# Kernel optimization log

Measured on AMD Instinct MI355X. Metric: run time of the kernel, lower is better.

The kernel has to match this reference:

```python
import jax, jax.numpy as jnp
import numpy as np

B, T, IN, H, OUT, L = 64, 4096, 32, 128, 32, 2


def setup_inputs() -> dict:
    key = jax.random.key(0)
    ks = jax.random.split(key, 12)
    s = 1.0 / np.sqrt(H)
    inp = {"x": jax.random.normal(ks[0], (B, T, IN), dtype=jnp.float32)}
    # layer 0 (input_dim -> H), layer 1 (H -> H); PyTorch GRU layout: [3H, in] with gates (r, z, n)
    inp["W_ih0"] = jax.random.uniform(ks[1], (3 * H, IN), jnp.float32, -s, s)
    inp["W_hh0"] = jax.random.uniform(ks[2], (3 * H, H), jnp.float32, -s, s)
    inp["b_ih0"] = jax.random.uniform(ks[3], (3 * H,), jnp.float32, -s, s)
    inp["b_hh0"] = jax.random.uniform(ks[4], (3 * H,), jnp.float32, -s, s)
    inp["W_ih1"] = jax.random.uniform(ks[5], (3 * H, H), jnp.float32, -s, s)
    inp["W_hh1"] = jax.random.uniform(ks[6], (3 * H, H), jnp.float32, -s, s)
    inp["b_ih1"] = jax.random.uniform(ks[7], (3 * H,), jnp.float32, -s, s)
    inp["b_hh1"] = jax.random.uniform(ks[8], (3 * H,), jnp.float32, -s, s)
    inp["fc_w"] = jax.random.uniform(ks[9], (OUT, H), jnp.float32, -s, s)
    inp["fc_b"] = jax.random.uniform(ks[10], (OUT,), jnp.float32, -s, s)
    return inp


def _gru_layer(x_seq, W_ih, W_hh, b_ih, b_hh):
    # x_seq: [B, T, in]; precompute the input projection as one big GEMM
    gi = jnp.einsum("bti,gi->btg", x_seq, W_ih) + b_ih  # [B, T, 3H]
    h0 = jnp.zeros((x_seq.shape[0], W_hh.shape[1]), x_seq.dtype)

    def step(h, gi_t):
        gh = h @ W_hh.T + b_hh  # [B, 3H]
        i_r, i_z, i_n = jnp.split(gi_t, 3, axis=-1)
        h_r, h_z, h_n = jnp.split(gh, 3, axis=-1)
        r = jax.nn.sigmoid(i_r + h_r)
        z = jax.nn.sigmoid(i_z + h_z)
        n = jnp.tanh(i_n + r * h_n)
        h_new = (1.0 - z) * n + z * h
        return h_new, h_new

    hT, outs = jax.lax.scan(step, h0, jnp.swapaxes(gi, 0, 1))  # outs: [T, B, H]
    return jnp.swapaxes(outs, 0, 1), hT


def reference(x, W_ih0, W_hh0, b_ih0, b_hh0, W_ih1, W_hh1, b_ih1, b_hh1, fc_w, fc_b):
    y0, h0 = _gru_layer(x, W_ih0, W_hh0, b_ih0, b_hh0)
    y1, h1 = _gru_layer(y0, W_ih1, W_hh1, b_ih1, b_hh1)
    out = jnp.einsum("bth,oh->bto", y1, fc_w) + fc_b  # [B, T, OUT]
    h = jnp.stack([h0, h1], axis=0)  # [n_layers, B, H]
    return out, h
```

## Files before the change

### kernel.cpp

```cpp
#include <hip/hip_runtime.h>

#define BB 64
#define TT 4096
#define IN0 32
#define HH 128
#define G3 384
#define NOUT 32
#define RING 64
#define CH 8

typedef _Float16 h2 __attribute__((ext_vector_type(2)));
typedef _Float16 h8 __attribute__((ext_vector_type(8)));
union H8 { h8 v; h2 p[4]; };

struct SM {
    float pg[G3 * 5];
    float pgi[G3 * 5];
    float hs[2][HH];
    _Float16 hf[2][HH];
    _Float16 xh[2][IN0];
    _Float16 ys[CH][HH];
    float bias1[G3];
    float bias2[G3];
    float fcw[NOUT * 129];
    float fcb[NOUT];
    float pfc[NOUT * 9];
};

__device__ __forceinline__ float fast_sigmoid(float x) {
    x = fminf(fmaxf(x, -30.f), 30.f);
    float e = __expf(-x);
    return __builtin_amdgcn_rcpf(1.f + e);
}
__device__ __forceinline__ float fast_tanh(float x) {
    x = fminf(fmaxf(x, -15.f), 15.f);
    float e = __expf(-2.f * x);
    return (1.f - e) * __builtin_amdgcn_rcpf(1.f + e);
}
__device__ __forceinline__ float fdot2(h2 a, h2 b, float c) {
#if __has_builtin(__builtin_amdgcn_fdot2)
    return __builtin_amdgcn_fdot2(a, b, c, false);
#else
    return fmaf((float)a.x, (float)b.x, fmaf((float)a.y, (float)b.y, c));
#endif
}
__device__ __forceinline__ int aload(const int* p) {
    return __hip_atomic_load(p, __ATOMIC_RELAXED, __HIP_MEMORY_SCOPE_AGENT);
}
__device__ __forceinline__ void astore(int* p, int v) {
    __hip_atomic_store(p, v, __ATOMIC_RELAXED, __HIP_MEMORY_SCOPE_AGENT);
}
__device__ __forceinline__ h2 cvt2(float a, float b) {
    h2 r; r.x = (_Float16)a; r.y = (_Float16)b; return r;
}

__device__ void role_A(SM& sm, const float* __restrict__ xb,
                       const float* __restrict__ W_ih, const float* __restrict__ W_hh,
                       const float* __restrict__ b_ih, const float* __restrict__ b_hh,
                       _Float16* __restrict__ y0b, float* __restrict__ hout, int* flagA)
{
    const int tid = threadIdx.x;
    const int rp = tid % 192, kq = tid / 192;
    const int r0 = 2 * rp, r1 = r0 + 1;
    const int pA0 = r0 * 5 + kq, pA1 = r1 * 5 + kq;

    h2 wh0[16], wh1[16], wi0[4], wi1[4];
    #pragma unroll
    for (int i = 0; i < 16; ++i) {
        float2 f0 = *(const float2*)&W_hh[r0 * HH + kq * 32 + 2 * i];
        float2 f1 = *(const float2*)&W_hh[r1 * HH + kq * 32 + 2 * i];
        wh0[i] = cvt2(f0.x, f0.y); wh1[i] = cvt2(f1.x, f1.y);
    }
    #pragma unroll
    for (int i = 0; i < 4; ++i) {
        float2 f0 = *(const float2*)&W_ih[r0 * IN0 + kq * 8 + 2 * i];
        float2 f1 = *(const float2*)&W_ih[r1 * IN0 + kq * 8 + 2 * i];
        wi0[i] = cvt2(f0.x, f0.y); wi1[i] = cvt2(f1.x, f1.y);
    }
    for (int i = tid; i < G3; i += 768) { sm.bias1[i] = b_ih[i]; sm.bias2[i] = b_hh[i]; }
    if (tid < HH) { sm.hs[0][tid] = 0.f; sm.hf[0][tid] = (_Float16)0.f; }
    if (tid < 8) {
        float4 f = ((const float4*)xb)[tid];
        ((h2*)&sm.xh[0][0])[2 * tid]     = cvt2(f.x, f.y);
        ((h2*)&sm.xh[0][0])[2 * tid + 1] = cvt2(f.z, f.w);
    }
    __syncthreads();

    int cur = 0;
    for (int t = 0; t < TT; ++t) {
        float4 pf;
        if (tid >= 128 && tid < 136) {
            int tn = (t + 1 < TT) ? t + 1 : t;
            pf = ((const float4*)(xb + (size_t)tn * IN0))[tid - 128];
        }
        const h8* hv = (const h8*)&sm.hf[cur][kq * 32];
        float a0 = 0.f, a1 = 0.f;
        #pragma unroll
        for (int i = 0; i < 4; ++i) {
            H8 hh; hh.v = hv[i];
            #pragma unroll
            for (int j = 0; j < 4; ++j) {
                a0 = fdot2(wh0[4 * i + j], hh.p[j], a0);
                a1 = fdot2(wh1[4 * i + j], hh.p[j], a1);
            }
        }
        sm.pg[pA0] = a0; sm.pg[pA1] = a1;
        H8 xx; xx.v = ((const h8*)&sm.xh[cur][0])[kq];
        float c0 = 0.f, c1 = 0.f;
        #pragma unroll
        for (int j = 0; j < 4; ++j) {
            c0 = fdot2(wi0[j], xx.p[j], c0);
            c1 = fdot2(wi1[j], xx.p[j], c1);
        }
        sm.pgi[pA0] = c0; sm.pgi[pA1] = c1;
        __syncthreads();

        const int nxt = cur ^ 1;
        if (tid < HH) {
            const int j = tid;
            float gir = sm.pgi[j*5+0]+sm.pgi[j*5+1]+sm.pgi[j*5+2]+sm.pgi[j*5+3] + sm.bias1[j];
            float giz = sm.pgi[(j+HH)*5+0]+sm.pgi[(j+HH)*5+1]+sm.pgi[(j+HH)*5+2]+sm.pgi[(j+HH)*5+3] + sm.bias1[j+HH];
            float gin = sm.pgi[(j+2*HH)*5+0]+sm.pgi[(j+2*HH)*5+1]+sm.pgi[(j+2*HH)*5+2]+sm.pgi[(j+2*HH)*5+3] + sm.bias1[j+2*HH];
            float ghr = sm.pg[j*5+0]+sm.pg[j*5+1]+sm.pg[j*5+2]+sm.pg[j*5+3] + sm.bias2[j];
            float ghz = sm.pg[(j+HH)*5+0]+sm.pg[(j+HH)*5+1]+sm.pg[(j+HH)*5+2]+sm.pg[(j+HH)*5+3] + sm.bias2[j+HH];
            float ghn = sm.pg[(j+2*HH)*5+0]+sm.pg[(j+2*HH)*5+1]+sm.pg[(j+2*HH)*5+2]+sm.pg[(j+2*HH)*5+3] + sm.bias2[j+2*HH];
            float rg = fast_sigmoid(gir + ghr);
            float zg = fast_sigmoid(giz + ghz);
            float ng = fast_tanh(gin + rg * ghn);
            float hn = (1.f - zg) * ng + zg * sm.hs[cur][j];
            sm.hs[nxt][j] = hn;
            sm.hf[nxt][j] = (_Float16)hn;
            y0b[(size_t)t * HH + j] = (_Float16)hn;
            if (t == TT - 1) hout[j] = hn;
        } else if (tid < 136) {
            int i = tid - 128;
            ((h2*)&sm.xh[nxt][0])[2 * i]     = cvt2(pf.x, pf.y);
            ((h2*)&sm.xh[nxt][0])[2 * i + 1] = cvt2(pf.z, pf.w);
        }
        __syncthreads();
        if ((t & 7) == 7 && tid == 0) { __threadfence(); astore(flagA, t + 1); }
        cur = nxt;
    }
}

__device__ void role_B(SM& sm, const _Float16* __restrict__ y0b,
                       const float* __restrict__ W_ih, const float* __restrict__ b_ih,
                       float* __restrict__ ring, int* flagA, int* flagB, int* flagC)
{
    const int tid = threadIdx.x;
    const int rp = tid % 192, kq = tid / 192;
    const int r0 = 2 * rp, r1 = r0 + 1;
    const int pA0 = r0 * 5 + kq, pA1 = r1 * 5 + kq;

    h2 wi0[16], wi1[16];
    #pragma unroll
    for (int i = 0; i < 16; ++i) {
        float2 f0 = *(const float2*)&W_ih[r0 * HH + kq * 32 + 2 * i];
        float2 f1 = *(const float2*)&W_ih[r1 * HH + kq * 32 + 2 * i];
        wi0[i] = cvt2(f0.x, f0.y); wi1[i] = cvt2(f1.x, f1.y);
    }
    for (int i = tid; i < G3; i += 768) sm.bias1[i] = b_ih[i];

    for (int T0 = 0; T0 < TT; T0 += CH) {
        if (tid == 0) {
            while (aload(flagA) < T0 + CH) __builtin_amdgcn_s_sleep(2);
            int need = T0 + CH - RING;
            while (aload(flagC) < need) __builtin_amdgcn_s_sleep(2);
            __threadfence();
        }
        __syncthreads();
        for (int i = tid; i < CH * HH / 2; i += 768)
            ((unsigned*)sm.ys)[i] = ((const unsigned*)(y0b + (size_t)T0 * HH))[i];
        __syncthreads();
        for (int s = 0; s < CH; ++s) {
            const h8* yv = (const h8*)&sm.ys[s][kq * 32];
            float a0 = 0.f, a1 = 0.f;
            #pragma unroll
            for (int i = 0; i < 4; ++i) {
                H8 yy; yy.v = yv[i];
                #pragma unroll
                for (int j = 0; j < 4; ++j) {
                    a0 = fdot2(wi0[4 * i + j], yy.p[j], a0);
                    a1 = fdot2(wi1[4 * i + j], yy.p[j], a1);
                }
            }
            sm.pg[pA0] = a0; sm.pg[pA1] = a1;
            __syncthreads();
            if (tid < G3) {
                float sum = sm.pg[tid*5+0]+sm.pg[tid*5+1]+sm.pg[tid*5+2]+sm.pg[tid*5+3] + sm.bias1[tid];
                ring[(size_t)((T0 + s) & (RING - 1)) * G3 + tid] = sum;
            }
            __syncthreads();
        }
        if (tid == 0) { __threadfence(); astore(flagB, T0 + CH); }
    }
}

__device__ void role_C(SM& sm, const float* __restrict__ ring,
                       const float* __restrict__ W_hh, const float* __restrict__ b_hh,
                       const float* __restrict__ fc_w, const float* __restrict__ fc_b,
                       float* __restrict__ outb, float* __restrict__ hout,
                       int* flagB, int* flagC)
{
    const int tid = threadIdx.x;
    const int rp = tid % 192, kq = tid / 192;
    const int r0 = 2 * rp, r1 = r0 + 1;
    const int pA0 = r0 * 5 + kq, pA1 = r1 * 5 + kq;

    h2 wh0[16], wh1[16];
    #pragma unroll
    for (int i = 0; i < 16; ++i) {
        float2 f0 = *(const float2*)&W_hh[r0 * HH + kq * 32 + 2 * i];
        float2 f1 = *(const float2*)&W_hh[r1 * HH + kq * 32 + 2 * i];
        wh0[i] = cvt2(f0.x, f0.y); wh1[i] = cvt2(f1.x, f1.y);
    }
    if (tid == 0) astore(flagC, 0);
    for (int i = tid; i < G3; i += 768) sm.bias2[i] = b_hh[i];
    for (int i = tid; i < NOUT * HH; i += 768)
        sm.fcw[(i >> 7) * 129 + (i & 127)] = fc_w[i];
    if (tid < NOUT) sm.fcb[tid] = fc_b[tid];
    if (tid < HH) { sm.hs[0][tid] = 0.f; sm.hf[0][tid] = (_Float16)0.f; }
    __syncthreads();

    int cur = 0;
    for (int t = 0; t < TT; ++t) {
        if ((t & 7) == 0) {
            if (tid == 0) {
                while (aload(flagB) < t + CH) __builtin_amdgcn_s_sleep(2);
                __threadfence();
            }
            __syncthreads();
        }
        if (t >= 2 && tid >= 704 && tid < 736) {
            int o = tid - 704;
            float s = sm.fcb[o];
            #pragma unroll
            for (int j = 0; j < 8; ++j) s += sm.pfc[o * 9 + j];
            outb[(size_t)(t - 2) * NOUT + o] = s;
        }
        float gir = 0.f, giz = 0.f, gin = 0.f;
        if (tid < HH) {
            const float* rr = ring + (size_t)(t & (RING - 1)) * G3;
            gir = rr[tid]; giz = rr[tid + HH]; gin = rr[tid + 2 * HH];
        }
        const h8* hv = (const h8*)&sm.hf[cur][kq * 32];
        float a0 = 0.f, a1 = 0.f;
        #pragma unroll
        for (int i = 0; i < 4; ++i) {
            H8 hh; hh.v = hv[i];
            #pragma unroll
            for (int j = 0; j < 4; ++j) {
                a0 = fdot2(wh0[4 * i + j], hh.p[j], a0);
                a1 = fdot2(wh1[4 * i + j], hh.p[j], a1);
            }
        }
        sm.pg[pA0] = a0; sm.pg[pA1] = a1;
        __syncthreads();

        const int nxt = cur ^ 1;
        if (tid < HH) {
            const int j = tid;
            float ghr = sm.pg[j*5+0]+sm.pg[j*5+1]+sm.pg[j*5+2]+sm.pg[j*5+3] + sm.bias2[j];
            float ghz = sm.pg[(j+HH)*5+0]+sm.pg[(j+HH)*5+1]+sm.pg[(j+HH)*5+2]+sm.pg[(j+HH)*5+3] + sm.bias2[j+HH];
            float ghn = sm.pg[(j+2*HH)*5+0]+sm.pg[(j+2*HH)*5+1]+sm.pg[(j+2*HH)*5+2]+sm.pg[(j+2*HH)*5+3] + sm.bias2[j+2*HH];
            float rg = fast_sigmoid(gir + ghr);
            float zg = fast_sigmoid(giz + ghz);
            float ng = fast_tanh(gin + rg * ghn);
            float hn = (1.f - zg) * ng + zg * sm.hs[cur][j];
            sm.hs[nxt][j] = hn;
            sm.hf[nxt][j] = (_Float16)hn;
            if (t == TT - 1) hout[j] = hn;
        }
        if (tid >= 384 && tid < 640) {
            int idx = tid - 384, o = idx & 31, ks = idx >> 5;
            const float* hv2 = &sm.hs[cur][ks * 16];
            const float* wv = &sm.fcw[o * 129 + ks * 16];
            float s = 0.f;
            #pragma unroll
            for (int i = 0; i < 16; ++i) s = fmaf(hv2[i], wv[i], s);
            sm.pfc[o * 9 + ks] = s;
        }
        __syncthreads();
        if ((t & 7) == 7 && tid == 0) { __threadfence(); astore(flagC, t + 1); }
        cur = nxt;
    }
    if (tid >= 704 && tid < 736) {
        int o = tid - 704;
        float s = sm.fcb[o];
        #pragma unroll
        for (int j = 0; j < 8; ++j) s += sm.pfc[o * 9 + j];
        outb[(size_t)(TT - 2) * NOUT + o] = s;
    }
    __syncthreads();
    if (tid >= 384 && tid < 640) {
        int idx = tid - 384, o = idx & 31, ks = idx >> 5;
        const float* hv2 = &sm.hs[cur][ks * 16];
        const float* wv = &sm.fcw[o * 129 + ks * 16];
        float s = 0.f;
        #pragma unroll
        for (int i = 0; i < 16; ++i) s = fmaf(hv2[i], wv[i], s);
        sm.pfc[o * 9 + ks] = s;
    }
    __syncthreads();
    if (tid >= 704 && tid < 736) {
        int o = tid - 704;
        float s = sm.fcb[o];
        #pragma unroll
        for (int j = 0; j < 8; ++j) s += sm.pfc[o * 9 + j];
        outb[(size_t)(TT - 1) * NOUT + o] = s;
    }
}

extern "C" __global__ void __launch_bounds__(768, 3)
gru_pipe_kernel(
    const float* x,
    const float* W_ih0, const float* W_hh0, const float* b_ih0, const float* b_hh0,
    const float* W_ih1, const float* W_hh1, const float* b_ih1, const float* b_hh1,
    const float* fc_w, const float* fc_b,
    float* out, float* hstack, _Float16* y0, float* ring, int* flags)
{
    __shared__ SM sm;
    const int wg = blockIdx.x;
    if (wg < BB) {
        const int b = wg;
        role_A(sm, x + (size_t)b * TT * IN0, W_ih0, W_hh0, b_ih0, b_hh0,
               y0 + (size_t)b * TT * HH, hstack + b * HH,
               &flags[(0 * 64 + b) * 16]);
    } else if (wg < 2 * BB) {
        const int b = wg - BB;
        role_B(sm, y0 + (size_t)b * TT * HH, W_ih1, b_ih1,
               ring + (size_t)b * RING * G3,
               &flags[(0 * 64 + b) * 16], &flags[(1 * 64 + b) * 16], &flags[(2 * 64 + b) * 16]);
    } else {
        const int b = wg - 2 * BB;
        role_C(sm, ring + (size_t)b * RING * G3, W_hh1, b_hh1, fc_w, fc_b,
               out + (size_t)b * TT * NOUT, hstack + BB * HH + b * HH,
               &flags[(1 * 64 + b) * 16], &flags[(2 * 64 + b) * 16]);
    }
}

extern "C" void kernel_launch(void* const* d_in, const int* in_sizes, int n_in,
                              void* d_out, int out_size, void* d_ws, size_t ws_size,
                              hipStream_t stream) {
    const float* x     = (const float*)d_in[0];
    const float* W_ih0 = (const float*)d_in[1];
    const float* W_hh0 = (const float*)d_in[2];
    const float* b_ih0 = (const float*)d_in[3];
    const float* b_hh0 = (const float*)d_in[4];
    const float* W_ih1 = (const float*)d_in[5];
    const float* W_hh1 = (const float*)d_in[6];
    const float* b_ih1 = (const float*)d_in[7];
    const float* b_hh1 = (const float*)d_in[8];
    const float* fc_w  = (const float*)d_in[9];
    const float* fc_b  = (const float*)d_in[10];

    float* out    = (float*)d_out;
    float* hstack = out + (size_t)BB * TT * NOUT;
    _Float16* y0  = (_Float16*)d_ws;
    float* ring   = (float*)((char*)d_ws + (68ull << 20));
    int* flags    = (int*)((char*)d_ws + (80ull << 20));

    gru_pipe_kernel<<<3 * BB, 768, 0, stream>>>(
        x, W_ih0, W_hh0, b_ih0, b_hh0,
        W_ih1, W_hh1, b_ih1, b_hh1,
        fc_w, fc_b, out, hstack, y0, ring, flags);
}
```

Measured before the change: 4.840 ms.

## Merge layer-1 input projection into recurrence block, one full gate row per thread

Removes the separate layer-1 input-projection role and its global ring buffer. Layer 1's recurrent blocks now compute both the W_ih and W_hh dot products themselves, reading y0 directly and waiting only on layer 0's progress flag. Each of 384 threads owns a full gate row, with 64 h2 weights held in registers per matrix, so the per-step K-split reduction through shared memory disappears. Block size drops from 768 to 384 threads and the grid from 192 to 128 blocks. The cost is much higher register pressure per thread and more serial dot-product work per thread on each step.

```diff
diff --git a/kernel.cpp b/kernel.cpp
--- a/kernel.cpp
+++ b/kernel.cpp
@@ -6,25 +6,18 @@
 #define HH 128
 #define G3 384
 #define NOUT 32
-#define RING 64
-#define CH 8
 
 typedef _Float16 h2 __attribute__((ext_vector_type(2)));
 typedef _Float16 h8 __attribute__((ext_vector_type(8)));
 union H8 { h8 v; h2 p[4]; };
 
 struct SM {
-    float pg[G3 * 5];
-    float pgi[G3 * 5];
+    float g[2 * HH];
+    float gin[HH];
+    float ghn[HH];
     float hs[2][HH];
     _Float16 hf[2][HH];
-    _Float16 xh[2][IN0];
-    _Float16 ys[CH][HH];
-    float bias1[G3];
-    float bias2[G3];
-    float fcw[NOUT * 129];
-    float fcb[NOUT];
-    float pfc[NOUT * 9];
+    float pfc[2][NOUT * 9];
 };
 
 __device__ __forceinline__ float fast_sigmoid(float x) {
@@ -60,282 +53,225 @@
                        _Float16* __restrict__ y0b, float* __restrict__ hout, int* flagA)
 {
     const int tid = threadIdx.x;
-    const int rp = tid % 192, kq = tid / 192;
-    const int r0 = 2 * rp, r1 = r0 + 1;
-    const int pA0 = r0 * 5 + kq, pA1 = r1 * 5 + kq;
-
-    h2 wh0[16], wh1[16], wi0[4], wi1[4];
-    #pragma unroll
-    for (int i = 0; i < 16; ++i) {
-        float2 f0 = *(const float2*)&W_hh[r0 * HH + kq * 32 + 2 * i];
-        float2 f1 = *(const float2*)&W_hh[r1 * HH + kq * 32 + 2 * i];
-        wh0[i] = cvt2(f0.x, f0.y); wh1[i] = cvt2(f1.x, f1.y);
-    }
-    #pragma unroll
-    for (int i = 0; i < 4; ++i) {
-        float2 f0 = *(const float2*)&W_ih[r0 * IN0 + kq * 8 + 2 * i];
-        float2 f1 = *(const float2*)&W_ih[r1 * IN0 + kq * 8 + 2 * i];
-        wi0[i] = cvt2(f0.x, f0.y); wi1[i] = cvt2(f1.x, f1.y);
-    }
-    for (int i = tid; i < G3; i += 768) { sm.bias1[i] = b_ih[i]; sm.bias2[i] = b_hh[i]; }
-    if (tid < HH) { sm.hs[0][tid] = 0.f; sm.hf[0][tid] = (_Float16)0.f; }
-    if (tid < 8) {
-        float4 f = ((const float4*)xb)[tid];
-        ((h2*)&sm.xh[0][0])[2 * tid]     = cvt2(f.x, f.y);
-        ((h2*)&sm.xh[0][0])[2 * tid + 1] = cvt2(f.z, f.w);
+    h2 wh[64], wi[16];
+    #pragma unroll
+    for (int k = 0; k < 64; ++k) {
+        float2 f = *(const float2*)&W_hh[tid * HH + 2 * k];
+        wh[k] = cvt2(f.x, f.y);
+    }
+    #pragma unroll
+    for (int k = 0; k < 16; ++k) {
+        float2 f = *(const float2*)&W_ih[tid * IN0 + 2 * k];
+        wi[k] = cvt2(f.x, f.y);
+    }
+    const bool is_n = tid >= 2 * HH;
+    const float bi = b_ih[tid], bh = b_hh[tid];
+    float hreg = 0.f;
+    if (tid < HH) sm.hf[0][tid] = (_Float16)0.f;
+
+    float4 pf[8];
+    #pragma unroll
+    for (int i = 0; i < 8; ++i) pf[i] = ((const float4*)xb)[i];
+    h2 xc[16];
+    #pragma unroll
+    for (int i = 0; i < 8; ++i) {
+        xc[2 * i]     = cvt2(pf[i].x, pf[i].y);
+        xc[2 * i + 1] = cvt2(pf[i].z, pf[i].w);
     }
     __syncthreads();
 
     int cur = 0;
     for (int t = 0; t < TT; ++t) {
-        float4 pf;
-        if (tid >= 128 && tid < 136) {
-            int tn = (t + 1 < TT) ? t + 1 : t;
-            pf = ((const float4*)(xb + (size_t)tn * IN0))[tid - 128];
-        }
-        const h8* hv = (const h8*)&sm.hf[cur][kq * 32];
-        float a0 = 0.f, a1 = 0.f;
-        #pragma unroll
-        for (int i = 0; i < 4; ++i) {
+        const int tn = (t + 1 < TT) ? t + 1 : t;
+        #pragma unroll
+        for (int i = 0; i < 8; ++i) pf[i] = ((const float4*)(xb + (size_t)tn * IN0))[i];
+
+        float ah0 = bh, ah1 = 0.f;
+        const h8* hv = (const h8*)&sm.hf[cur][0];
+        #pragma unroll
+        for (int i = 0; i < 16; ++i) {
             H8 hh; hh.v = hv[i];
             #pragma unroll
             for (int j = 0; j < 4; ++j) {
-                a0 = fdot2(wh0[4 * i + j], hh.p[j], a0);
-                a1 = fdot2(wh1[4 * i + j], hh.p[j], a1);
+                if (((4 * i + j) & 1) == 0) ah0 = fdot2(wh[4 * i + j], hh.p[j], ah0);
+                else                        ah1 = fdot2(wh[4 * i + j], hh.p[j], ah1);
             }
         }
-        sm.pg[pA0] = a0; sm.pg[pA1] = a1;
-        H8 xx; xx.v = ((const h8*)&sm.xh[cur][0])[kq];
-        float c0 = 0.f, c1 = 0.f;
-        #pragma unroll
-        for (int j = 0; j < 4; ++j) {
-            c0 = fdot2(wi0[j], xx.p[j], c0);
-            c1 = fdot2(wi1[j], xx.p[j], c1);
-        }
-        sm.pgi[pA0] = c0; sm.pgi[pA1] = c1;
+        float ai0 = bi, ai1 = 0.f;
+        #pragma unroll
+        for (int j = 0; j < 16; ++j) {
+            if (j & 1) ai1 = fdot2(wi[j], xc[j], ai1);
+            else       ai0 = fdot2(wi[j], xc[j], ai0);
+        }
+        const float sgh = ah0 + ah1, sgi = ai0 + ai1;
+        if (!is_n) sm.g[tid] = sgh + sgi;
+        else { sm.gin[tid - 2 * HH] = sgi; sm.ghn[tid - 2 * HH] = sgh; }
         __syncthreads();
 
-        const int nxt = cur ^ 1;
         if (tid < HH) {
-            const int j = tid;
-            float gir = sm.pgi[j*5+0]+sm.pgi[j*5+1]+sm.pgi[j*5+2]+sm.pgi[j*5+3] + sm.bias1[j];
-            float giz = sm.pgi[(j+HH)*5+0]+sm.pgi[(j+HH)*5+1]+sm.pgi[(j+HH)*5+2]+sm.pgi[(j+HH)*5+3] + sm.bias1[j+HH];
-            float gin = sm.pgi[(j+2*HH)*5+0]+sm.pgi[(j+2*HH)*5+1]+sm.pgi[(j+2*HH)*5+2]+sm.pgi[(j+2*HH)*5+3] + sm.bias1[j+2*HH];
-            float ghr = sm.pg[j*5+0]+sm.pg[j*5+1]+sm.pg[j*5+2]+sm.pg[j*5+3] + sm.bias2[j];
-            float ghz = sm.pg[(j+HH)*5+0]+sm.pg[(j+HH)*5+1]+sm.pg[(j+HH)*5+2]+sm.pg[(j+HH)*5+3] + sm.bias2[j+HH];
-            float ghn = sm.pg[(j+2*HH)*5+0]+sm.pg[(j+2*HH)*5+1]+sm.pg[(j+2*HH)*5+2]+sm.pg[(j+2*HH)*5+3] + sm.bias2[j+2*HH];
-            float rg = fast_sigmoid(gir + ghr);
-            float zg = fast_sigmoid(giz + ghz);
-            float ng = fast_tanh(gin + rg * ghn);
-            float hn = (1.f - zg) * ng + zg * sm.hs[cur][j];
-            sm.hs[nxt][j] = hn;
-            sm.hf[nxt][j] = (_Float16)hn;
-            y0b[(size_t)t * HH + j] = (_Float16)hn;
-            if (t == TT - 1) hout[j] = hn;
-        } else if (tid < 136) {
-            int i = tid - 128;
-            ((h2*)&sm.xh[nxt][0])[2 * i]     = cvt2(pf.x, pf.y);
-            ((h2*)&sm.xh[nxt][0])[2 * i + 1] = cvt2(pf.z, pf.w);
+            float rg = fast_sigmoid(sm.g[tid]);
+            float zg = fast_sigmoid(sm.g[tid + HH]);
+            float ng = fast_tanh(sm.gin[tid] + rg * sm.ghn[tid]);
+            hreg = (1.f - zg) * ng + zg * hreg;
+            sm.hf[cur ^ 1][tid] = (_Float16)hreg;
+            y0b[(size_t)t * HH + tid] = (_Float16)hreg;
+            if (t == TT - 1) hout[tid] = hreg;
+        }
+        #pragma unroll
+        for (int i = 0; i < 8; ++i) {
+            xc[2 * i]     = cvt2(pf[i].x, pf[i].y);
+            xc[2 * i + 1] = cvt2(pf[i].z, pf[i].w);
         }
         __syncthreads();
         if ((t & 7) == 7 && tid == 0) { __threadfence(); astore(flagA, t + 1); }
-        cur = nxt;
-    }
-}
-
-__device__ void role_B(SM& sm, const _Float16* __restrict__ y0b,
-                       const float* __restrict__ W_ih, const float* __restrict__ b_ih,
-                       float* __restrict__ ring, int* flagA, int* flagB, int* flagC)
+        cur ^= 1;
+    }
+}
+
+__device__ void role_C(SM& sm, const _Float16* __restrict__ yb,
+                       const float* __restrict__ W_ih, const float* __restrict__ W_hh,
+                       const float* __restrict__ b_ih, const float* __restrict__ b_hh,
+                       const float* __restrict__ fc_w, const float* __restrict__ fc_b,
+                       float* __restrict__ outb, float* __restrict__ hout, int* flagA)
 {
     const int tid = threadIdx.x;
-    const int rp = tid % 192, kq = tid / 192;
-    const int r0 = 2 * rp, r1 = r0 + 1;
-    const int pA0 = r0 * 5 + kq, pA1 = r1 * 5 + kq;
-
-    h2 wi0[16], wi1[16];
-    #pragma unroll
-    for (int i = 0; i < 16; ++i) {
-        float2 f0 = *(const float2*)&W_ih[r0 * HH + kq * 32 + 2 * i];
-        float2 f1 = *(const float2*)&W_ih[r1 * HH + kq * 32 + 2 * i];
-        wi0[i] = cvt2(f0.x, f0.y); wi1[i] = cvt2(f1.x, f1.y);
-    }
-    for (int i = tid; i < G3; i += 768) sm.bias1[i] = b_ih[i];
-
-    for (int T0 = 0; T0 < TT; T0 += CH) {
-        if (tid == 0) {
-            while (aload(flagA) < T0 + CH) __builtin_amdgcn_s_sleep(2);
-            int need = T0 + CH - RING;
-            while (aload(flagC) < need) __builtin_amdgcn_s_sleep(2);
-            __threadfence();
-        }
-        __syncthreads();
-        for (int i = tid; i < CH * HH / 2; i += 768)
-            ((unsigned*)sm.ys)[i] = ((const unsigned*)(y0b + (size_t)T0 * HH))[i];
-        __syncthreads();
-        for (int s = 0; s < CH; ++s) {
-            const h8* yv = (const h8*)&sm.ys[s][kq * 32];
-            float a0 = 0.f, a1 = 0.f;
-            #pragma unroll
-            for (int i = 0; i < 4; ++i) {
-                H8 yy; yy.v = yv[i];
-                #pragma unroll
-                for (int j = 0; j < 4; ++j) {
-                    a0 = fdot2(wi0[4 * i + j], yy.p[j], a0);
-                    a1 = fdot2(wi1[4 * i + j], yy.p[j], a1);
-                }
-            }
-            sm.pg[pA0] = a0; sm.pg[pA1] = a1;
-            __syncthreads();
-            if (tid < G3) {
-                float sum = sm.pg[tid*5+0]+sm.pg[tid*5+1]+sm.pg[tid*5+2]+sm.pg[tid*5+3] + sm.bias1[tid];
-                ring[(size_t)((T0 + s) & (RING - 1)) * G3 + tid] = sum;
-            }
-            __syncthreads();
-        }
-        if (tid == 0) { __threadfence(); astore(flagB, T0 + CH); }
-    }
-}
-
-__device__ void role_C(SM& sm, const float* __restrict__ ring,
-                       const float* __restrict__ W_hh, const float* __restrict__ b_hh,
-                       const float* __restrict__ fc_w, const float* __restrict__ fc_b,
-                       float* __restrict__ outb, float* __restrict__ hout,
-                       int* flagB, int* flagC)
-{
-    const int tid = threadIdx.x;
-    const int rp = tid % 192, kq = tid / 192;
-    const int r0 = 2 * rp, r1 = r0 + 1;
-    const int pA0 = r0 * 5 + kq, pA1 = r1 * 5 + kq;
-
-    h2 wh0[16], wh1[16];
-    #pragma unroll
-    for (int i = 0; i < 16; ++i) {
-        float2 f0 = *(const float2*)&W_hh[r0 * HH + kq * 32 + 2 * i];
-        float2 f1 = *(const float2*)&W_hh[r1 * HH + kq * 32 + 2 * i];
-        wh0[i] = cvt2(f0.x, f0.y); wh1[i] = cvt2(f1.x, f1.y);
-    }
-    if (tid == 0) astore(flagC, 0);
-    for (int i = tid; i < G3; i += 768) sm.bias2[i] = b_hh[i];
-    for (int i = tid; i < NOUT * HH; i += 768)
-        sm.fcw[(i >> 7) * 129 + (i & 127)] = fc_w[i];
-    if (tid < NOUT) sm.fcb[tid] = fc_b[tid];
-    if (tid < HH) { sm.hs[0][tid] = 0.f; sm.hf[0][tid] = (_Float16)0.f; }
+    h2 wh[64], wi[64];
+    #pragma unroll
+    for (int k = 0; k < 64; ++k) {
+        float2 f = *(const float2*)&W_hh[tid * HH + 2 * k]; wh[k] = cvt2(f.x, f.y);
+        float2 g = *(const float2*)&W_ih[tid * HH + 2 * k]; wi[k] = cvt2(g.x, g.y);
+    }
+    const bool is_n = tid >= 2 * HH;
+    const float bi = b_ih[tid], bh = b_hh[tid];
+    float hreg = 0.f;
+    const int fidx = tid - HH, fo = fidx & 31, fks = fidx >> 5;
+    float fw[16]; float fb = 0.f;
+    if (tid >= HH) {
+        #pragma unroll
+        for (int i = 0; i < 16; ++i) fw[i] = fc_w[fo * HH + fks * 16 + i];
+        if (tid < HH + NOUT) fb = fc_b[fo];
+    }
+    if (tid < HH) { sm.hf[0][tid] = (_Float16)0.f; sm.hs[0][tid] = 0.f; sm.hs[1][tid] = 0.f; }
+
+    if (tid == 0) {
+        while (aload(flagA) < 16) __builtin_amdgcn_s_sleep(8);
+        __threadfence();
+    }
     __syncthreads();
+    H8 yv[16];
+    #pragma unroll
+    for (int i = 0; i < 16; ++i) yv[i].v = ((const h8*)yb)[i];
 
     int cur = 0;
     for (int t = 0; t < TT; ++t) {
-        if ((t & 7) == 0) {
+        if (t && (t & 7) == 0) {
             if (tid == 0) {
-                while (aload(flagB) < t + CH) __builtin_amdgcn_s_sleep(2);
+                int tgt = t + 16; if (tgt > TT) tgt = TT;
+                while (aload(flagA) < tgt) __builtin_amdgcn_s_sleep(2);
                 __threadfence();
             }
             __syncthreads();
         }
-        if (t >= 2 && tid >= 704 && tid < 736) {
-            int o = tid - 704;
-            float s = sm.fcb[o];
-            #pragma unroll
-            for (int j = 0; j < 8; ++j) s += sm.pfc[o * 9 + j];
-            outb[(size_t)(t - 2) * NOUT + o] = s;
-        }
-        float gir = 0.f, giz = 0.f, gin = 0.f;
+
+        float ah0 = bh, ah1 = 0.f;
+        const h8* hv = (const h8*)&sm.hf[cur][0];
+        #pragma unroll
+        for (int i = 0; i < 16; ++i) {
+            H8 hh; hh.v = hv[i];
+            #pragma unroll
+            for (int j = 0; j < 4; ++j) {
+                if (((4 * i + j) & 1) == 0) ah0 = fdot2(wh[4 * i + j], hh.p[j], ah0);
+                else                        ah1 = fdot2(wh[4 * i + j], hh.p[j], ah1);
+            }
+        }
+        float ai0 = bi, ai1 = 0.f;
+        #pragma unroll
+        for (int i = 0; i < 16; ++i) {
+            #pragma unroll
+            for (int j = 0; j < 4; ++j) {
+                if (((4 * i + j) & 1) == 0) ai0 = fdot2(wi[4 * i + j], yv[i].p[j], ai0);
+                else                        ai1 = fdot2(wi[4 * i + j], yv[i].p[j], ai1);
+            }
+        }
+        const int tn = (t + 1 < TT) ? t + 1 : t;
+        const h8* ysrc = (const h8*)(yb + (size_t)tn * HH);
+        #pragma unroll
+        for (int i = 0; i < 16; ++i) yv[i].v = ysrc[i];
+
+        const float sgh = ah0 + ah1, sgi = ai0 + ai1;
+        if (!is_n) sm.g[tid] = sgh + sgi;
+        else { sm.gin[tid - 2 * HH] = sgi; sm.ghn[tid - 2 * HH] = sgh; }
+
+        if (tid >= HH) {
+            const float* hvv = &sm.hs[cur][fks * 16];
+            float s = 0.f;
+            #pragma unroll
+            for (int i = 0; i < 16; ++i) s = fmaf(fw[i], hvv[i], s);
+            sm.pfc[t & 1][fo * 9 + fks] = s;
+        }
+        if (t >= 2 && tid >= HH && tid < HH + NOUT) {
+            float s = fb;
+            #pragma unroll
+            for (int j = 0; j < 8; ++j) s += sm.pfc[(t - 1) & 1][fo * 9 + j];
+            outb[(size_t)(t - 2) * NOUT + fo] = s;
+        }
+        __syncthreads();
+
         if (tid < HH) {
-            const float* rr = ring + (size_t)(t & (RING - 1)) * G3;
-            gir = rr[tid]; giz = rr[tid + HH]; gin = rr[tid + 2 * HH];
-        }
-        const h8* hv = (const h8*)&sm.hf[cur][kq * 32];
-        float a0 = 0.f, a1 = 0.f;
-        #pragma unroll
-        for (int i = 0; i < 4; ++i) {
-            H8 hh; hh.v = hv[i];
-            #pragma unroll
-            for (int j = 0; j < 4; ++j) {
-                a0 = fdot2(wh0[4 * i + j], hh.p[j], a0);
-                a1 = fdot2(wh1[4 * i + j], hh.p[j], a1);
-            }
-        }
-        sm.pg[pA0] = a0; sm.pg[pA1] = a1;
+            float rg = fast_sigmoid(sm.g[tid]);
+            float zg = fast_sigmoid(sm.g[tid + HH]);
+            float ng = fast_tanh(sm.gin[tid] + rg * sm.ghn[tid]);
+            hreg = (1.f - zg) * ng + zg * hreg;
+            sm.hf[cur ^ 1][tid] = (_Float16)hreg;
+            sm.hs[cur ^ 1][tid] = hreg;
+            if (t == TT - 1) hout[tid] = hreg;
+        }
         __syncthreads();
-
-        const int nxt = cur ^ 1;
-        if (tid < HH) {
-            const int j = tid;
-            float ghr = sm.pg[j*5+0]+sm.pg[j*5+1]+sm.pg[j*5+2]+sm.pg[j*5+3] + sm.bias2[j];
-            float ghz = sm.pg[(j+HH)*5+0]+sm.pg[(j+HH)*5+1]+sm.pg[(j+HH)*5+2]+sm.pg[(j+HH)*5+3] + sm.bias2[j+HH];
-            float ghn = sm.pg[(j+2*HH)*5+0]+sm.pg[(j+2*HH)*5+1]+sm.pg[(j+2*HH)*5+2]+sm.pg[(j+2*HH)*5+3] + sm.bias2[j+2*HH];
-            float rg = fast_sigmoid(gir + ghr);
-            float zg = fast_sigmoid(giz + ghz);
-            float ng = fast_tanh(gin + rg * ghn);
-            float hn = (1.f - zg) * ng + zg * sm.hs[cur][j];
-            sm.hs[nxt][j] = hn;
-            sm.hf[nxt][j] = (_Float16)hn;
-            if (t == TT - 1) hout[j] = hn;
-        }
-        if (tid >= 384 && tid < 640) {
-            int idx = tid - 384, o = idx & 31, ks = idx >> 5;
-            const float* hv2 = &sm.hs[cur][ks * 16];
-            const float* wv = &sm.fcw[o * 129 + ks * 16];
-            float s = 0.f;
-            #pragma unroll
-            for (int i = 0; i < 16; ++i) s = fmaf(hv2[i], wv[i], s);
-            sm.pfc[o * 9 + ks] = s;
-        }
-        __syncthreads();
-        if ((t & 7) == 7 && tid == 0) { __threadfence(); astore(flagC, t + 1); }
-        cur = nxt;
-    }
-    if (tid >= 704 && tid < 736) {
-        int o = tid - 704;
-        float s = sm.fcb[o];
-        #pragma unroll
-        for (int j = 0; j < 8; ++j) s += sm.pfc[o * 9 + j];
-        outb[(size_t)(TT - 2) * NOUT + o] = s;
+        cur ^= 1;
+    }
+
+    if (tid >= HH && tid < HH + NOUT) {
+        float s = fb;
+        #pragma unroll
+        for (int j = 0; j < 8; ++j) s += sm.pfc[(TT - 1) & 1][fo * 9 + j];
+        outb[(size_t)(TT - 2) * NOUT + fo] = s;
+    }
+    if (tid >= HH) {
+        const float* hvv = &sm.hs[cur][fks * 16];
+        float s = 0.f;
+        #pragma unroll
+        for (int i = 0; i < 16; ++i) s = fmaf(fw[i], hvv[i], s);
+        sm.pfc[TT & 1][fo * 9 + fks] = s;
     }
     __syncthreads();
-    if (tid >= 384 && tid < 640) {
-        int idx = tid - 384, o = idx & 31, ks = idx >> 5;
-        const float* hv2 = &sm.hs[cur][ks * 16];
-        const float* wv = &sm.fcw[o * 129 + ks * 16];
-        float s = 0.f;
-        #pragma unroll
-        for (int i = 0; i < 16; ++i) s = fmaf(hv2[i], wv[i], s);
-        sm.pfc[o * 9 + ks] = s;
-    }
-    __syncthreads();
-    if (tid >= 704 && tid < 736) {
-        int o = tid - 704;
-        float s = sm.fcb[o];
-        #pragma unroll
-        for (int j = 0; j < 8; ++j) s += sm.pfc[o * 9 + j];
-        outb[(size_t)(TT - 1) * NOUT + o] = s;
-    }
-}
-
-extern "C" __global__ void __launch_bounds__(768, 3)
-gru_pipe_kernel(
+    if (tid >= HH && tid < HH + NOUT) {
+        float s = fb;
+        #pragma unroll
+        for (int j = 0; j < 8; ++j) s += sm.pfc[TT & 1][fo * 9 + j];
+        outb[(size_t)(TT - 1) * NOUT + fo] = s;
+    }
+}
+
+extern "C" __global__ void __launch_bounds__(384, 1)
+__attribute__((amdgpu_waves_per_eu(1, 2)))
+gru2_kernel(
     const float* x,
     const float* W_ih0, const float* W_hh0, const float* b_ih0, const float* b_hh0,
     const float* W_ih1, const float* W_hh1, const float* b_ih1, const float* b_hh1,
     const float* fc_w, const float* fc_b,
-    float* out, float* hstack, _Float16* y0, float* ring, int* flags)
+    float* out, float* hstack, _Float16* y0, int* flags)
 {
     __shared__ SM sm;
     const int wg = blockIdx.x;
     if (wg < BB) {
         const int b = wg;
         role_A(sm, x + (size_t)b * TT * IN0, W_ih0, W_hh0, b_ih0, b_hh0,
-               y0 + (size_t)b * TT * HH, hstack + b * HH,
-               &flags[(0 * 64 + b) * 16]);
-    } else if (wg < 2 * BB) {
+               y0 + (size_t)b * TT * HH, hstack + b * HH, flags + b * 16);
+    } else {
         const int b = wg - BB;
-        role_B(sm, y0 + (size_t)b * TT * HH, W_ih1, b_ih1,
-               ring + (size_t)b * RING * G3,
-               &flags[(0 * 64 + b) * 16], &flags[(1 * 64 + b) * 16], &flags[(2 * 64 + b) * 16]);
-    } else {
-        const int b = wg - 2 * BB;
-        role_C(sm, ring + (size_t)b * RING * G3, W_hh1, b_hh1, fc_w, fc_b,
-               out + (size_t)b * TT * NOUT, hstack + BB * HH + b * HH,
-               &flags[(1 * 64 + b) * 16], &flags[(2 * 64 + b) * 16]);
+        role_C(sm, y0 + (size_t)b * TT * HH, W_ih1, W_hh1, b_ih1, b_hh1,
+               fc_w, fc_b, out + (size_t)b * TT * NOUT,
+               hstack + BB * HH + b * HH, flags + b * 16);
     }
 }
 
@@ -357,11 +293,10 @@
     float* out    = (float*)d_out;
     float* hstack = out + (size_t)BB * TT * NOUT;
     _Float16* y0  = (_Float16*)d_ws;
-    float* ring   = (float*)((char*)d_ws + (68ull << 20));
     int* flags    = (int*)((char*)d_ws + (80ull << 20));
 
-    gru_pipe_kernel<<<3 * BB, 768, 0, stream>>>(
+    gru2_kernel<<<2 * BB, 384, 0, stream>>>(
         x, W_ih0, W_hh0, b_ih0, b_hh0,
         W_ih1, W_hh1, b_ih1, b_hh1,
-        fc_w, fc_b, out, hstack, y0, ring, flags);
-}
+        fc_w, fc_b, out, hstack, y0, flags);
+}
```

New measurement: 6.260 ms. +29.4%, slower.
